# Performance work log

Hardware: AMD Instinct MI355X
Metric: run time of the kernel (lower is better)

Reference implementation:

```python
import jax, jax.numpy as jnp
import numpy as np

B, W, NN, EPG = 8, 16, 64, 1024   # batch, window, nodes/graph, trace-edges/graph
N = B * W * NN                     # 8192 flattened nodes
E = B * W * EPG                    # 131072 node-graph edges == trace rows
E2 = 4 * E                         # 524288 edge-graph (line-graph) edges
D_NODE = 128; D_LOG = 128; D_EDGE = 128
D_IN = D_NODE + D_LOG              # 256 = GATv2 node2node in_channels
H = 4
EPS = 1e-16                        # PyG softmax epsilon


def _lin(key, fan_in, fan_out):
    return jax.random.normal(key, (fan_in, fan_out), jnp.float32) * (1.0 / np.sqrt(fan_in))


def setup_inputs() -> dict:
    key = jax.random.key(0)
    ks = jax.random.split(key, 16)
    return {
        "x_node": jax.random.normal(ks[0], (B, W, NN, D_NODE), jnp.float32),
        "x_trace": jax.random.normal(ks[1], (B, W, EPG, D_EDGE), jnp.float32),
        "x_log": jax.random.normal(ks[2], (B, W, NN, D_LOG), jnp.float32),
        "node_adj": jax.random.randint(ks[3], (2, E), 0, N, jnp.int32),
        "edge_adj": jax.random.randint(ks[4], (2, E2), 0, E, jnp.int32),
        "edge_efea": jax.random.randint(ks[5], (E2,), 0, N, jnp.int32),
        # node2node GATv2Conv: in=256, heads=4, out/head=64, edge_dim=128
        "n2n_Wl": _lin(ks[6], D_IN, D_IN), "n2n_bl": jnp.zeros((D_IN,), jnp.float32),
        "n2n_Wr": _lin(ks[7], D_IN, D_IN), "n2n_br": jnp.zeros((D_IN,), jnp.float32),
        "n2n_We": _lin(ks[8], D_EDGE, D_IN),
        "n2n_att": jax.random.normal(ks[9], (H, D_IN // H), jnp.float32) * 0.1,
        "n2n_bias": jnp.zeros((D_IN,), jnp.float32),
        # egde2node GATv2Conv: in=128, heads=4, out/head=32, edge_dim=256
        "e2n_Wl": _lin(ks[10], D_EDGE, D_EDGE), "e2n_bl": jnp.zeros((D_EDGE,), jnp.float32),
        "e2n_Wr": _lin(ks[11], D_EDGE, D_EDGE), "e2n_br": jnp.zeros((D_EDGE,), jnp.float32),
        "e2n_We": _lin(ks[12], D_IN, D_EDGE),
        "e2n_att": jax.random.normal(ks[13], (H, D_EDGE // H), jnp.float32) * 0.1,
        "e2n_bias": jnp.zeros((D_EDGE,), jnp.float32),
    }


def gatv2(x, edge_index, edge_attr, Wl, bl, Wr, br, We, att, bias, num_nodes):
    """PyG GATv2Conv (eval mode, add_self_loops=False, concat heads)."""
    heads, C = att.shape
    src, dst = edge_index[0], edge_index[1]
    xl = (x @ Wl + bl).reshape(-1, heads, C)   # source transform [N,H,C]
    xr = (x @ Wr + br).reshape(-1, heads, C)   # target transform [N,H,C]
    e = (edge_attr @ We).reshape(-1, heads, C) # edge transform   [E,H,C]
    m = jax.nn.leaky_relu(xl[src] + xr[dst] + e, 0.2)  # [E,H,C]
    alpha = jnp.einsum('ehc,hc->eh', m, att)           # [E,H]
    amax = jax.ops.segment_max(alpha, dst, num_segments=num_nodes)
    ex = jnp.exp(alpha - amax[dst])
    denom = jax.ops.segment_sum(ex, dst, num_segments=num_nodes)
    a = ex / (denom[dst] + EPS)                        # per-target softmax
    out = jax.ops.segment_sum(a[:, :, None] * xl[src], dst, num_segments=num_nodes)
    return out.reshape(num_nodes, heads * C) + bias


def reference(x_node, x_trace, x_log, node_adj, edge_adj, edge_efea,
              n2n_Wl, n2n_bl, n2n_Wr, n2n_br, n2n_We, n2n_att, n2n_bias,
              e2n_Wl, e2n_bl, e2n_Wr, e2n_br, e2n_We, e2n_att, e2n_bias):
    node = jnp.concatenate([x_node, x_log], axis=-1).reshape(-1, D_IN)  # [N,256]
    trace = x_trace.reshape(-1, D_EDGE)                                 # [E,128]
    node = gatv2(node, node_adj, trace,
                 n2n_Wl, n2n_bl, n2n_Wr, n2n_br, n2n_We, n2n_att, n2n_bias, N)
    trace = gatv2(trace, edge_adj, node[edge_efea],
                  e2n_Wl, e2n_bl, e2n_Wr, e2n_br, e2n_We, e2n_att, e2n_bias, E)
    xn = node[:, :D_NODE].reshape(B, W, NN, D_NODE)
    xt = trace.reshape(B, W, EPG, D_EDGE)
    xlg = node[:, D_NODE:].reshape(B, W, NN, D_LOG)
    return (xn, xt, xlg)
```

## Files before the change

### kernel.cpp

```cpp
#include <hip/hip_runtime.h>
#include <hip/hip_bf16.h>

constexpr int N    = 8192;
constexpr int E    = 131072;
constexpr int E2   = 524288;

constexpr size_t XT_OFF  = (size_t)N * 128;
constexpr size_t XLG_OFF = XT_OFF + (size_t)E * 128;

typedef unsigned short u16;
typedef short s16x8 __attribute__((ext_vector_type(8)));
typedef float f32x4 __attribute__((ext_vector_type(4)));

__device__ __forceinline__ u16 f2bs(float f) {
    unsigned x = __float_as_uint(f);
    return (u16)((x + 0x7FFF + ((x >> 16) & 1)) >> 16);
}
__device__ __forceinline__ float bs2f(u16 u) {
    return __uint_as_float((unsigned)u << 16);
}

__global__ __launch_bounds__(256) void k_prep(
    const float* __restrict__ Wl, const float* __restrict__ Wr,
    const float* __restrict__ We, const float* __restrict__ Wl2,
    const float* __restrict__ Wr2, const float* __restrict__ We2,
    u16* __restrict__ Wlt, u16* __restrict__ Wrt, u16* __restrict__ Wet,
    u16* __restrict__ Wl2t, u16* __restrict__ Wr2t, u16* __restrict__ We2t)
{
    const int gid = blockIdx.x * 256 + threadIdx.x;
    const float* src; u16* dst; int base, Kk, sh, perm;
    if      (gid <  65536) { src = Wl;  dst = Wlt;  base = 0;      Kk = 256; sh = 8; perm = 0; }
    else if (gid < 131072) { src = Wr;  dst = Wrt;  base = 65536;  Kk = 256; sh = 8; perm = 0; }
    else if (gid < 163840) { src = We;  dst = Wet;  base = 131072; Kk = 128; sh = 8; perm = 1; }
    else if (gid < 180224) { src = Wl2; dst = Wl2t; base = 163840; Kk = 128; sh = 7; perm = 1; }
    else if (gid < 196608) { src = Wr2; dst = Wr2t; base = 180224; Kk = 128; sh = 7; perm = 1; }
    else                   { src = We2; dst = We2t; base = 196608; Kk = 256; sh = 7; perm = 0; }
    const int l = gid - base;
    const int k = l >> sh, nn = l & ((1 << sh) - 1);
    int ns = nn;
    if (perm) ns = (nn & ~63) | ((nn & 3) << 4) | ((nn >> 2) & 15);
    dst[(size_t)ns * Kk + k] = f2bs(src[l]);
}

__global__ void k_hist(const int* __restrict__ dst, int* __restrict__ cnt, int nE)
{
    int i = blockIdx.x * 256 + threadIdx.x;
    if (i < nE) atomicAdd(&cnt[dst[i]], 1);
}

__global__ __launch_bounds__(1024) void k_scan(
    const int* __restrict__ cnt, int* __restrict__ off, int* __restrict__ cur, int n)
{
    __shared__ int tile[8192];
    __shared__ int wsum[16];
    const int tid = threadIdx.x, lane = tid & 63, wv = tid >> 6;
    int carry = 0;
    for (int base = 0; base < n; base += 8192) {
        for (int i = tid; i < 8192; i += 1024) tile[i] = cnt[base + i];
        __syncthreads();
        const int st = tid * 8;
        int s = 0;
        for (int k = 0; k < 8; ++k) { int v = tile[st + k]; tile[st + k] = s; s += v; }
        const int tsum = s;
        int incl = s;
        for (int o = 1; o < 64; o <<= 1) {
            int v = __shfl_up(incl, o);
            if (lane >= o) incl += v;
        }
        if (lane == 63) wsum[wv] = incl;
        __syncthreads();
        int woff = 0;
        for (int wq = 0; wq < wv; ++wq) woff += wsum[wq];
        int tot = 0;
        for (int wq = 0; wq < 16; ++wq) tot += wsum[wq];
        const int add = carry + woff + incl - tsum;
        for (int k = 0; k < 8; ++k) {
            int o2 = add + tile[st + k];
            off[base + st + k] = o2;
            cur[base + st + k] = o2;
        }
        carry += tot;
        __syncthreads();
    }
    if (tid == 0) off[n] = carry;
}

__global__ void k_scatter1(const int* __restrict__ adj, int* __restrict__ cur,
                           int* __restrict__ srcc, int* __restrict__ pos1, int nE)
{
    int i = blockIdx.x * 256 + threadIdx.x;
    if (i < nE) {
        int pos = atomicAdd(&cur[adj[nE + i]], 1);
        srcc[pos] = adj[i];
        pos1[i] = pos;
    }
}

__global__ void k_scatter2(const int* __restrict__ eadj, const int* __restrict__ efea,
                           int* __restrict__ cur, int2* __restrict__ sf2, int nE)
{
    int i = blockIdx.x * 256 + threadIdx.x;
    if (i < nE) {
        int pos = atomicAdd(&cur[eadj[nE + i]], 1);
        sf2[pos] = make_int2(eadj[i], efea[i]);
    }
}

__global__ __launch_bounds__(256) void k_node_gemm(
    const float* __restrict__ x_node, const float* __restrict__ x_log,
    const u16* __restrict__ Wlt, const float* __restrict__ bl,
    const u16* __restrict__ Wrt, const float* __restrict__ br,
    u16* __restrict__ xl, u16* __restrict__ xr)
{
    __shared__ u16 A[32][260];
    const int n0 = blockIdx.x * 32;
    const int tid = threadIdx.x;
    for (int i = tid; i < 32 * 64; i += 256) {
        const int r = i >> 6, k4 = (i & 63) << 2;
        const float* srcp = (k4 < 128) ? &x_node[(size_t)(n0 + r) * 128 + k4]
                                       : &x_log [(size_t)(n0 + r) * 128 + (k4 - 128)];
        const float4 v = *(const float4*)srcp;
        ushort4 o; o.x = f2bs(v.x); o.y = f2bs(v.y); o.z = f2bs(v.z); o.w = f2bs(v.w);
        *(ushort4*)&A[r][k4] = o;
    }
    __syncthreads();
    const int w = tid >> 6, lane = tid & 63, lr = lane & 15, lq = lane >> 4;
    const u16* Wt     = (w < 2) ? Wlt : Wrt;
    const float* bias = (w < 2) ? bl : br;
    u16* outp         = (w < 2) ? xl : xr;
    const int cb = (w & 1) * 128;
    f32x4 acc[2][8] = {};
    for (int kb = 0; kb < 8; ++kb) {
        s16x8 afr0 = *(const s16x8*)&A[lr][kb * 32 + lq * 8];
        s16x8 afr1 = *(const s16x8*)&A[16 + lr][kb * 32 + lq * 8];
#pragma unroll
        for (int ct = 0; ct < 8; ++ct) {
            const int n = cb + ct * 16 + lr;
            s16x8 bfr = *(const s16x8*)&Wt[(size_t)n * 256 + kb * 32 + lq * 8];
            acc[0][ct] = __builtin_amdgcn_mfma_f32_16x16x32_bf16(afr0, bfr, acc[0][ct], 0, 0, 0);
            acc[1][ct] = __builtin_amdgcn_mfma_f32_16x16x32_bf16(afr1, bfr, acc[1][ct], 0, 0, 0);
        }
    }
#pragma unroll
    for (int rt = 0; rt < 2; ++rt)
#pragma unroll
        for (int ct = 0; ct < 8; ++ct) {
            const int col = cb + ct * 16 + lr;
            const float bv = bias[col];
#pragma unroll
            for (int reg = 0; reg < 4; ++reg) {
                const int row = n0 + rt * 16 + lq * 4 + reg;
                outp[(size_t)row * 256 + col] = f2bs(acc[rt][ct][reg] + bv);
            }
        }
}

__global__ __launch_bounds__(512) void k_edge_mm(
    const float* __restrict__ x_trace,
    const int* __restrict__ adj,
    const int* __restrict__ pos1,
    const u16* __restrict__ xl_n, const u16* __restrict__ xr_n,
    const u16* __restrict__ Wet,
    const u16* __restrict__ Wl2t, const float* __restrict__ bl2,
    const u16* __restrict__ Wr2t, const float* __restrict__ br2,
    const float* __restrict__ att,
    float* __restrict__ alpha, u16* __restrict__ xl_e, u16* __restrict__ xrst)
{
    __shared__ u16 A[32][132];
    __shared__ int ss[32], dd[32], pp[32];
    const int e0 = blockIdx.x * 32;
    const int tid = threadIdx.x;
    for (int i = tid; i < 32 * 32; i += 512) {
        const int r = i >> 5, k4 = (i & 31) << 2;
        const float4 v = *(const float4*)&x_trace[(size_t)(e0 + r) * 128 + k4];
        ushort4 o; o.x = f2bs(v.x); o.y = f2bs(v.y); o.z = f2bs(v.z); o.w = f2bs(v.w);
        *(ushort4*)&A[r][k4] = o;
    }
    if (tid < 32) {
        ss[tid] = adj[e0 + tid];
        dd[tid] = adj[E + e0 + tid];
        pp[tid] = pos1[e0 + tid];
    }
    __syncthreads();
    const int w8 = tid >> 6;
    const int role = w8 >> 2;
    const int w = w8 & 3;
    const int lane = tid & 63, lr = lane & 15, lq = lane >> 4;

    if (role == 0) {
        const int co = w * 64 + lr * 4;
        ushort4 xlv[2][4], xrv[2][4];
#pragma unroll
        for (int rt = 0; rt < 2; ++rt)
#pragma unroll
            for (int reg = 0; reg < 4; ++reg) {
                const int rowt = rt * 16 + lq * 4 + reg;
                xlv[rt][reg] = *(const ushort4*)&xl_n[(size_t)ss[rowt] * 256 + co];
                xrv[rt][reg] = *(const ushort4*)&xr_n[(size_t)dd[rowt] * 256 + co];
            }
        f32x4 acc1[2][4] = {};
        for (int kb = 0; kb < 4; ++kb) {
            s16x8 afr0 = *(const s16x8*)&A[lr][kb * 32 + lq * 8];
            s16x8 afr1 = *(const s16x8*)&A[16 + lr][kb * 32 + lq * 8];
#pragma unroll
            for (int ct = 0; ct < 4; ++ct) {
                const int n1 = w * 64 + ct * 16 + lr;
                s16x8 bfr = *(const s16x8*)&Wet[(size_t)n1 * 128 + kb * 32 + lq * 8];
                acc1[0][ct] = __builtin_amdgcn_mfma_f32_16x16x32_bf16(afr0, bfr, acc1[0][ct], 0, 0, 0);
                acc1[1][ct] = __builtin_amdgcn_mfma_f32_16x16x32_bf16(afr1, bfr, acc1[1][ct], 0, 0, 0);
            }
        }
        const float4 attq = *(const float4*)&att[w * 64 + lr * 4];
        float sums[2][4];
#pragma unroll
        for (int rt = 0; rt < 2; ++rt)
#pragma unroll
            for (int reg = 0; reg < 4; ++reg) {
                float m0 = acc1[rt][0][reg] + bs2f(xlv[rt][reg].x) + bs2f(xrv[rt][reg].x);
                float m1 = acc1[rt][1][reg] + bs2f(xlv[rt][reg].y) + bs2f(xrv[rt][reg].y);
                float m2 = acc1[rt][2][reg] + bs2f(xlv[rt][reg].z) + bs2f(xrv[rt][reg].z);
                float m3 = acc1[rt][3][reg] + bs2f(xlv[rt][reg].w) + bs2f(xrv[rt][reg].w);
                m0 = m0 > 0.f ? m0 : 0.2f * m0;
                m1 = m1 > 0.f ? m1 : 0.2f * m1;
                m2 = m2 > 0.f ? m2 : 0.2f * m2;
                m3 = m3 > 0.f ? m3 : 0.2f * m3;
                sums[rt][reg] = m0 * attq.x + m1 * attq.y + m2 * attq.z + m3 * attq.w;
            }
#pragma unroll
        for (int rt = 0; rt < 2; ++rt)
#pragma unroll
            for (int reg = 0; reg < 4; ++reg) {
                float p = sums[rt][reg];
                p += __shfl_xor(p, 8);
                p += __shfl_xor(p, 4);
                p += __shfl_xor(p, 2);
                p += __shfl_xor(p, 1);
                if (lr == 0)
                    alpha[(size_t)pp[rt * 16 + lq * 4 + reg] * 4 + w] = p;
            }
    } else {
        const u16* Wt2  = (w < 2) ? Wl2t : Wr2t;
        const float* b2 = (w < 2) ? bl2 : br2;
        const int cb2 = (w & 1) * 64;
        f32x4 acc2[2][4] = {};
        for (int kb = 0; kb < 4; ++kb) {
            s16x8 afr0 = *(const s16x8*)&A[lr][kb * 32 + lq * 8];
            s16x8 afr1 = *(const s16x8*)&A[16 + lr][kb * 32 + lq * 8];
#pragma unroll
            for (int ct = 0; ct < 4; ++ct) {
                const int n2 = cb2 + ct * 16 + lr;
                s16x8 bfr = *(const s16x8*)&Wt2[(size_t)n2 * 128 + kb * 32 + lq * 8];
                acc2[0][ct] = __builtin_amdgcn_mfma_f32_16x16x32_bf16(afr0, bfr, acc2[0][ct], 0, 0, 0);
                acc2[1][ct] = __builtin_amdgcn_mfma_f32_16x16x32_bf16(afr1, bfr, acc2[1][ct], 0, 0, 0);
            }
        }
        const float4 b2q = *(const float4*)&b2[cb2 + lr * 4];
#pragma unroll
        for (int rt = 0; rt < 2; ++rt)
#pragma unroll
            for (int reg = 0; reg < 4; ++reg) {
                const int row = e0 + rt * 16 + lq * 4 + reg;
                ushort4 o;
                o.x = f2bs(acc2[rt][0][reg] + b2q.x);
                o.y = f2bs(acc2[rt][1][reg] + b2q.y);
                o.z = f2bs(acc2[rt][2][reg] + b2q.z);
                o.w = f2bs(acc2[rt][3][reg] + b2q.w);
                if (w < 2) *(ushort4*)&xl_e[(size_t)row * 128 + cb2 + lr * 4] = o;
                else       *(ushort4*)&xrst[(size_t)row * 256 + cb2 + lr * 4] = o;
            }
    }
}

__global__ __launch_bounds__(256) void k_fused1(
    const int* __restrict__ off, const int* __restrict__ srcc,
    const float* __restrict__ alphac,
    const u16* __restrict__ xl,
    const float* __restrict__ bias,
    float* __restrict__ out)
{
    const int wv = __builtin_amdgcn_readfirstlane(threadIdx.x >> 6);
    const int lane = threadIdx.x & 63;
    const int n = blockIdx.x * 4 + wv;
    const int c = lane * 4;
    const int h = lane >> 4;
    const int beg = off[n], end = off[n + 1];
    float mx = -INFINITY, den = 0.f;
    float a0 = 0.f, a1 = 0.f, a2 = 0.f, a3 = 0.f;
    int i = beg;
    while (i < end) {
        const int rem = end - i;
        int sa[8]; float pe[8];
#pragma unroll
        for (int k = 0; k < 8; ++k) {
            const int idx = i + (k < rem ? k : rem - 1);
            sa[k] = srcc[idx];
            pe[k] = alphac[(size_t)idx * 4 + h];
        }
        ushort4 xv[8];
#pragma unroll
        for (int k = 0; k < 8; ++k)
            xv[k] = *(const ushort4*)&xl[(size_t)sa[k] * 256 + c];
#pragma unroll
        for (int k = 0; k < 8; ++k) {
            const float p = (k < rem) ? pe[k] : -INFINITY;
            const float mnew = fmaxf(mx, p);
            const float sc = __expf(mx - mnew);
            const float ex = __expf(p - mnew);
            den = den * sc + ex;
            a0 = a0 * sc + ex * bs2f(xv[k].x);
            a1 = a1 * sc + ex * bs2f(xv[k].y);
            a2 = a2 * sc + ex * bs2f(xv[k].z);
            a3 = a3 * sc + ex * bs2f(xv[k].w);
            mx = mnew;
        }
        i += 8;
    }
    const float inv = 1.f / (den + 1e-16f);
    float4 r;
    r.x = a0 * inv + bias[c + 0];
    r.y = a1 * inv + bias[c + 1];
    r.z = a2 * inv + bias[c + 2];
    r.w = a3 * inv + bias[c + 3];
    if (lane < 32) *(float4*)&out[(size_t)n * 128 + c] = r;
    else           *(float4*)&out[XLG_OFF + (size_t)n * 128 + (c - 128)] = r;
}

__global__ __launch_bounds__(256) void k_proj_gemm(
    const float* __restrict__ out_node, const u16* __restrict__ We2t,
    u16* __restrict__ proj)
{
    __shared__ u16 A[32][260];
    const int n0 = blockIdx.x * 32;
    const int tid = threadIdx.x;
    for (int i = tid; i < 32 * 64; i += 256) {
        const int r = i >> 6, k4 = (i & 63) << 2;
        const float* srcp = (k4 < 128)
            ? &out_node[(size_t)(n0 + r) * 128 + k4]
            : &out_node[XLG_OFF + (size_t)(n0 + r) * 128 + (k4 - 128)];
        const float4 v = *(const float4*)srcp;
        ushort4 o; o.x = f2bs(v.x); o.y = f2bs(v.y); o.z = f2bs(v.z); o.w = f2bs(v.w);
        *(ushort4*)&A[r][k4] = o;
    }
    __syncthreads();
    const int w = tid >> 6, lane = tid & 63, lr = lane & 15, lq = lane >> 4;
    f32x4 acc[2][2] = {};
    for (int kb = 0; kb < 8; ++kb) {
        s16x8 afr0 = *(const s16x8*)&A[lr][kb * 32 + lq * 8];
        s16x8 afr1 = *(const s16x8*)&A[16 + lr][kb * 32 + lq * 8];
#pragma unroll
        for (int ct = 0; ct < 2; ++ct) {
            const int col = w * 32 + ct * 16 + lr;
            s16x8 bfr = *(const s16x8*)&We2t[(size_t)col * 256 + kb * 32 + lq * 8];
            acc[0][ct] = __builtin_amdgcn_mfma_f32_16x16x32_bf16(afr0, bfr, acc[0][ct], 0, 0, 0);
            acc[1][ct] = __builtin_amdgcn_mfma_f32_16x16x32_bf16(afr1, bfr, acc[1][ct], 0, 0, 0);
        }
    }
#pragma unroll
    for (int rt = 0; rt < 2; ++rt)
#pragma unroll
        for (int ct = 0; ct < 2; ++ct) {
            const int col = w * 32 + ct * 16 + lr;
#pragma unroll
            for (int reg = 0; reg < 4; ++reg) {
                const int row = n0 + rt * 16 + lq * 4 + reg;
                proj[(size_t)row * 128 + col] = f2bs(acc[rt][ct][reg]);
            }
        }
}

__global__ __launch_bounds__(256) void k_fused2(
    const int* __restrict__ off, const int2* __restrict__ sf2,
    const u16* __restrict__ xl,
    const u16* __restrict__ proj,
    const float* __restrict__ att,
    const float* __restrict__ bias,
    float* __restrict__ out)
{
    const int wv = __builtin_amdgcn_readfirstlane(threadIdx.x >> 6);
    const int lane = threadIdx.x & 63;
    const int d = blockIdx.x * 4 + wv;
    const int c = lane * 2;
    const u16* xrst = (const u16*)(out + XT_OFF);
    const unsigned xrp = *(const unsigned*)&xrst[(size_t)d * 256 + c];
    const float xr0 = bs2f((u16)(xrp & 0xffff));
    const float xr1 = bs2f((u16)(xrp >> 16));
    const float av0 = att[c], av1 = att[c + 1];
    const int beg = off[d], end = off[d + 1];
    float mx = -INFINITY, den = 0.f, a0 = 0.f, a1 = 0.f;
    int i = beg;
    while (i < end) {
        const int rem = end - i;
        int2 sf[4];
#pragma unroll
        for (int k = 0; k < 4; ++k) sf[k] = sf2[i + (k < rem ? k : rem - 1)];
        unsigned xv[4], pv[4];
#pragma unroll
        for (int k = 0; k < 4; ++k) {
            xv[k] = *(const unsigned*)&xl[(size_t)sf[k].x * 128 + c];
            pv[k] = *(const unsigned*)&proj[(size_t)sf[k].y * 128 + c];
        }
#pragma unroll
        for (int k = 0; k < 4; ++k) {
            const float x0 = bs2f((u16)(xv[k] & 0xffff));
            const float x1 = bs2f((u16)(xv[k] >> 16));
            float m0 = x0 + xr0 + bs2f((u16)(pv[k] & 0xffff));
            float m1 = x1 + xr1 + bs2f((u16)(pv[k] >> 16));
            m0 = m0 > 0.f ? m0 : 0.2f * m0;
            m1 = m1 > 0.f ? m1 : 0.2f * m1;
            float pp = m0 * av0 + m1 * av1;
            pp += __shfl_xor(pp, 8, 16);
            pp += __shfl_xor(pp, 4, 16);
            pp += __shfl_xor(pp, 2, 16);
            pp += __shfl_xor(pp, 1, 16);
            const float p = (k < rem) ? pp : -INFINITY;
            const float mnew = fmaxf(mx, p);
            const float sc = __expf(mx - mnew);
            const float ex = __expf(p - mnew);
            den = den * sc + ex;
            a0 = a0 * sc + ex * x0;
            a1 = a1 * sc + ex * x1;
            mx = mnew;
        }
        i += 4;
    }
    const float inv = 1.f / (den + 1e-16f);
    float2 o2;
    o2.x = a0 * inv + bias[c];
    o2.y = a1 * inv + bias[c + 1];
    *(float2*)&out[XT_OFF + (size_t)d * 128 + c] = o2;
}

extern "C" void kernel_launch(void* const* d_in, const int* in_sizes, int n_in,
                              void* d_out, int out_size, void* d_ws, size_t ws_size,
                              hipStream_t stream)
{
    const float* x_node   = (const float*)d_in[0];
    const float* x_trace  = (const float*)d_in[1];
    const float* x_log    = (const float*)d_in[2];
    const int*   node_adj = (const int*)d_in[3];
    const int*   edge_adj = (const int*)d_in[4];
    const int*   efea     = (const int*)d_in[5];
    const float* n2n_Wl   = (const float*)d_in[6];
    const float* n2n_bl   = (const float*)d_in[7];
    const float* n2n_Wr   = (const float*)d_in[8];
    const float* n2n_br   = (const float*)d_in[9];
    const float* n2n_We   = (const float*)d_in[10];
    const float* n2n_att  = (const float*)d_in[11];
    const float* n2n_bias = (const float*)d_in[12];
    const float* e2n_Wl   = (const float*)d_in[13];
    const float* e2n_bl   = (const float*)d_in[14];
    const float* e2n_Wr   = (const float*)d_in[15];
    const float* e2n_br   = (const float*)d_in[16];
    const float* e2n_We   = (const float*)d_in[17];
    const float* e2n_att  = (const float*)d_in[18];
    const float* e2n_bias = (const float*)d_in[19];
    float* out = (float*)d_out;

    char* w = (char*)d_ws;
    int*  cnt1   = (int*)w;   w += (size_t)N * 4;
    int*  cnt2   = (int*)w;   w += (size_t)E * 4;
    int*  off1   = (int*)w;   w += (size_t)(N + 4) * 4;
    int*  cur1   = (int*)w;   w += (size_t)N * 4;
    int*  src1   = (int*)w;   w += (size_t)E * 4;
    int*  pos1   = (int*)w;   w += (size_t)E * 4;
    float* alphac = (float*)w; w += (size_t)E * 4 * 4;
    int*  off2   = (int*)w;   w += (size_t)(E + 4) * 4;
    int*  cur2   = (int*)w;   w += (size_t)E * 4;
    int2* sf2    = (int2*)w;  w += (size_t)E2 * 8;
    u16*  xl_n   = (u16*)w;   w += (size_t)N * 256 * 2;
    u16*  xr_n   = (u16*)w;   w += (size_t)N * 256 * 2;
    u16*  xl_e   = (u16*)w;   w += (size_t)E * 128 * 2;
    u16*  proj   = (u16*)w;   w += (size_t)N * 128 * 2;
    u16*  Wlt    = (u16*)w;   w += (size_t)65536 * 2;
    u16*  Wrt    = (u16*)w;   w += (size_t)65536 * 2;
    u16*  Wet    = (u16*)w;   w += (size_t)32768 * 2;
    u16*  Wl2t   = (u16*)w;   w += (size_t)16384 * 2;
    u16*  Wr2t   = (u16*)w;   w += (size_t)16384 * 2;
    u16*  We2t   = (u16*)w;   w += (size_t)32768 * 2;

    hipMemsetAsync(d_ws, 0, (size_t)(N + E) * 4, stream);

    k_prep<<<896, 256, 0, stream>>>(n2n_Wl, n2n_Wr, n2n_We, e2n_Wl, e2n_Wr, e2n_We,
                                    Wlt, Wrt, Wet, Wl2t, Wr2t, We2t);
    k_hist<<<E / 256, 256, 0, stream>>>(node_adj + E, cnt1, E);
    k_scan<<<1, 1024, 0, stream>>>(cnt1, off1, cur1, N);
    k_scatter1<<<E / 256, 256, 0, stream>>>(node_adj, cur1, src1, pos1, E);
    k_hist<<<E2 / 256, 256, 0, stream>>>(edge_adj + E2, cnt2, E2);
    k_scan<<<1, 1024, 0, stream>>>(cnt2, off2, cur2, E);
    k_scatter2<<<E2 / 256, 256, 0, stream>>>(edge_adj, efea, cur2, sf2, E2);

    k_node_gemm<<<N / 32, 256, 0, stream>>>(x_node, x_log, Wlt, n2n_bl, Wrt, n2n_br,
                                            xl_n, xr_n);
    k_edge_mm<<<E / 32, 512, 0, stream>>>(x_trace, node_adj, pos1, xl_n, xr_n,
                                          Wet, Wl2t, e2n_bl, Wr2t, e2n_br,
                                          n2n_att, alphac, xl_e, (u16*)(out + XT_OFF));
    k_fused1<<<N / 4, 256, 0, stream>>>(off1, src1, alphac, xl_n, n2n_bias, out);

    k_proj_gemm<<<N / 32, 256, 0, stream>>>(out, We2t, proj);
    k_fused2<<<E / 4, 256, 0, stream>>>(off2, sf2, xl_e, proj,
                                        e2n_att, e2n_bias, out);
}
```

Baseline: 453.8 us.

## Make edge GEMM kernel persistent over 8 tiles with double-buffered LDS and register-cached weights

Each block of k_edge_mm now handles 8 consecutive 32-edge tiles instead of one. The weight fragments are loaded into registers once per block instead of being re-read from global memory for every tile. The next tile's x_trace rows and indices are staged into a second LDS buffer while the current tile computes. This cuts repeated weight traffic and overlaps loads with MFMA work, but the grid shrinks to 512 blocks and register pressure rises from the 64 cached weight vectors per thread.

```diff
diff --git a/kernel.cpp b/kernel.cpp
--- a/kernel.cpp
+++ b/kernel.cpp
@@ -155,6 +155,7 @@
         }
 }
 
+constexpr int TPB_EDGE = 8;
 __global__ __launch_bounds__(512) void k_edge_mm(
     const float* __restrict__ x_trace,
     const int* __restrict__ adj,
@@ -166,108 +167,159 @@
     const float* __restrict__ att,
     float* __restrict__ alpha, u16* __restrict__ xl_e, u16* __restrict__ xrst)
 {
-    __shared__ u16 A[32][132];
-    __shared__ int ss[32], dd[32], pp[32];
-    const int e0 = blockIdx.x * 32;
+    __shared__ u16 A[2][32][132];
+    __shared__ int ss[2][32], dd[2][32], pp[2][32];
     const int tid = threadIdx.x;
-    for (int i = tid; i < 32 * 32; i += 512) {
-        const int r = i >> 5, k4 = (i & 31) << 2;
-        const float4 v = *(const float4*)&x_trace[(size_t)(e0 + r) * 128 + k4];
-        ushort4 o; o.x = f2bs(v.x); o.y = f2bs(v.y); o.z = f2bs(v.z); o.w = f2bs(v.w);
-        *(ushort4*)&A[r][k4] = o;
-    }
-    if (tid < 32) {
-        ss[tid] = adj[e0 + tid];
-        dd[tid] = adj[E + e0 + tid];
-        pp[tid] = pos1[e0 + tid];
-    }
-    __syncthreads();
     const int w8 = tid >> 6;
     const int role = w8 >> 2;
     const int w = w8 & 3;
     const int lane = tid & 63, lr = lane & 15, lq = lane >> 4;
 
+    s16x8 wf[4][4];
+    const int cb2 = (w & 1) * 64;
     if (role == 0) {
-        const int co = w * 64 + lr * 4;
-        ushort4 xlv[2][4], xrv[2][4];
-#pragma unroll
-        for (int rt = 0; rt < 2; ++rt)
-#pragma unroll
-            for (int reg = 0; reg < 4; ++reg) {
-                const int rowt = rt * 16 + lq * 4 + reg;
-                xlv[rt][reg] = *(const ushort4*)&xl_n[(size_t)ss[rowt] * 256 + co];
-                xrv[rt][reg] = *(const ushort4*)&xr_n[(size_t)dd[rowt] * 256 + co];
-            }
-        f32x4 acc1[2][4] = {};
-        for (int kb = 0; kb < 4; ++kb) {
-            s16x8 afr0 = *(const s16x8*)&A[lr][kb * 32 + lq * 8];
-            s16x8 afr1 = *(const s16x8*)&A[16 + lr][kb * 32 + lq * 8];
-#pragma unroll
-            for (int ct = 0; ct < 4; ++ct) {
-                const int n1 = w * 64 + ct * 16 + lr;
-                s16x8 bfr = *(const s16x8*)&Wet[(size_t)n1 * 128 + kb * 32 + lq * 8];
-                acc1[0][ct] = __builtin_amdgcn_mfma_f32_16x16x32_bf16(afr0, bfr, acc1[0][ct], 0, 0, 0);
-                acc1[1][ct] = __builtin_amdgcn_mfma_f32_16x16x32_bf16(afr1, bfr, acc1[1][ct], 0, 0, 0);
-            }
-        }
-        const float4 attq = *(const float4*)&att[w * 64 + lr * 4];
-        float sums[2][4];
-#pragma unroll
-        for (int rt = 0; rt < 2; ++rt)
-#pragma unroll
-            for (int reg = 0; reg < 4; ++reg) {
-                float m0 = acc1[rt][0][reg] + bs2f(xlv[rt][reg].x) + bs2f(xrv[rt][reg].x);
-                float m1 = acc1[rt][1][reg] + bs2f(xlv[rt][reg].y) + bs2f(xrv[rt][reg].y);
-                float m2 = acc1[rt][2][reg] + bs2f(xlv[rt][reg].z) + bs2f(xrv[rt][reg].z);
-                float m3 = acc1[rt][3][reg] + bs2f(xlv[rt][reg].w) + bs2f(xrv[rt][reg].w);
-                m0 = m0 > 0.f ? m0 : 0.2f * m0;
-                m1 = m1 > 0.f ? m1 : 0.2f * m1;
-                m2 = m2 > 0.f ? m2 : 0.2f * m2;
-                m3 = m3 > 0.f ? m3 : 0.2f * m3;
-                sums[rt][reg] = m0 * attq.x + m1 * attq.y + m2 * attq.z + m3 * attq.w;
-            }
-#pragma unroll
-        for (int rt = 0; rt < 2; ++rt)
-#pragma unroll
-            for (int reg = 0; reg < 4; ++reg) {
-                float p = sums[rt][reg];
-                p += __shfl_xor(p, 8);
-                p += __shfl_xor(p, 4);
-                p += __shfl_xor(p, 2);
-                p += __shfl_xor(p, 1);
-                if (lr == 0)
-                    alpha[(size_t)pp[rt * 16 + lq * 4 + reg] * 4 + w] = p;
-            }
+#pragma unroll
+        for (int kb = 0; kb < 4; ++kb)
+#pragma unroll
+            for (int ct = 0; ct < 4; ++ct)
+                wf[kb][ct] = *(const s16x8*)&Wet[(size_t)(w * 64 + ct * 16 + lr) * 128 + kb * 32 + lq * 8];
     } else {
-        const u16* Wt2  = (w < 2) ? Wl2t : Wr2t;
-        const float* b2 = (w < 2) ? bl2 : br2;
-        const int cb2 = (w & 1) * 64;
-        f32x4 acc2[2][4] = {};
-        for (int kb = 0; kb < 4; ++kb) {
-            s16x8 afr0 = *(const s16x8*)&A[lr][kb * 32 + lq * 8];
-            s16x8 afr1 = *(const s16x8*)&A[16 + lr][kb * 32 + lq * 8];
-#pragma unroll
-            for (int ct = 0; ct < 4; ++ct) {
-                const int n2 = cb2 + ct * 16 + lr;
-                s16x8 bfr = *(const s16x8*)&Wt2[(size_t)n2 * 128 + kb * 32 + lq * 8];
-                acc2[0][ct] = __builtin_amdgcn_mfma_f32_16x16x32_bf16(afr0, bfr, acc2[0][ct], 0, 0, 0);
-                acc2[1][ct] = __builtin_amdgcn_mfma_f32_16x16x32_bf16(afr1, bfr, acc2[1][ct], 0, 0, 0);
-            }
-        }
-        const float4 b2q = *(const float4*)&b2[cb2 + lr * 4];
-#pragma unroll
-        for (int rt = 0; rt < 2; ++rt)
-#pragma unroll
-            for (int reg = 0; reg < 4; ++reg) {
-                const int row = e0 + rt * 16 + lq * 4 + reg;
-                ushort4 o;
-                o.x = f2bs(acc2[rt][0][reg] + b2q.x);
-                o.y = f2bs(acc2[rt][1][reg] + b2q.y);
-                o.z = f2bs(acc2[rt][2][reg] + b2q.z);
-                o.w = f2bs(acc2[rt][3][reg] + b2q.w);
-                if (w < 2) *(ushort4*)&xl_e[(size_t)row * 128 + cb2 + lr * 4] = o;
-                else       *(ushort4*)&xrst[(size_t)row * 256 + cb2 + lr * 4] = o;
-            }
+        const u16* Wt2 = (w < 2) ? Wl2t : Wr2t;
+#pragma unroll
+        for (int kb = 0; kb < 4; ++kb)
+#pragma unroll
+            for (int ct = 0; ct < 4; ++ct)
+                wf[kb][ct] = *(const s16x8*)&Wt2[(size_t)(cb2 + ct * 16 + lr) * 128 + kb * 32 + lq * 8];
+    }
+    const float4 attq = *(const float4*)&att[w * 64 + lr * 4];
+    const float4 b2q  = (role == 0) ? make_float4(0, 0, 0, 0)
+        : *(const float4*)&((w < 2) ? bl2 : br2)[cb2 + lr * 4];
+
+    const int tile0 = blockIdx.x * TPB_EDGE;
+    {
+        const int e0s = tile0 * 32;
+        const int i0 = tid, i1 = tid + 512;
+        {
+            const int r = i0 >> 5, k4 = (i0 & 31) << 2;
+            const float4 v = *(const float4*)&x_trace[(size_t)(e0s + r) * 128 + k4];
+            ushort4 o; o.x = f2bs(v.x); o.y = f2bs(v.y); o.z = f2bs(v.z); o.w = f2bs(v.w);
+            *(ushort4*)&A[0][r][k4] = o;
+        }
+        {
+            const int r = i1 >> 5, k4 = (i1 & 31) << 2;
+            const float4 v = *(const float4*)&x_trace[(size_t)(e0s + r) * 128 + k4];
+            ushort4 o; o.x = f2bs(v.x); o.y = f2bs(v.y); o.z = f2bs(v.z); o.w = f2bs(v.w);
+            *(ushort4*)&A[0][r][k4] = o;
+        }
+        if (tid < 32) {
+            ss[0][tid] = adj[e0s + tid];
+            dd[0][tid] = adj[E + e0s + tid];
+            pp[0][tid] = pos1[e0s + tid];
+        }
+    }
+
+    for (int t = 0; t < TPB_EDGE; ++t) {
+        __syncthreads();
+        const int b = t & 1;
+        const int e0 = (tile0 + t) * 32;
+        if (t + 1 < TPB_EDGE) {
+            const int e0s = (tile0 + t + 1) * 32;
+            const int bn = b ^ 1;
+            {
+                const int r = tid >> 5, k4 = (tid & 31) << 2;
+                const float4 v = *(const float4*)&x_trace[(size_t)(e0s + r) * 128 + k4];
+                ushort4 o; o.x = f2bs(v.x); o.y = f2bs(v.y); o.z = f2bs(v.z); o.w = f2bs(v.w);
+                *(ushort4*)&A[bn][r][k4] = o;
+            }
+            {
+                const int i1 = tid + 512;
+                const int r = i1 >> 5, k4 = (i1 & 31) << 2;
+                const float4 v = *(const float4*)&x_trace[(size_t)(e0s + r) * 128 + k4];
+                ushort4 o; o.x = f2bs(v.x); o.y = f2bs(v.y); o.z = f2bs(v.z); o.w = f2bs(v.w);
+                *(ushort4*)&A[bn][r][k4] = o;
+            }
+            if (tid < 32) {
+                ss[bn][tid] = adj[e0s + tid];
+                dd[bn][tid] = adj[E + e0s + tid];
+                pp[bn][tid] = pos1[e0s + tid];
+            }
+        }
+
+        if (role == 0) {
+            const int co = w * 64 + lr * 4;
+            ushort4 xlv[2][4], xrv[2][4];
+#pragma unroll
+            for (int rt = 0; rt < 2; ++rt)
+#pragma unroll
+                for (int reg = 0; reg < 4; ++reg) {
+                    const int rowt = rt * 16 + lq * 4 + reg;
+                    xlv[rt][reg] = *(const ushort4*)&xl_n[(size_t)ss[b][rowt] * 256 + co];
+                    xrv[rt][reg] = *(const ushort4*)&xr_n[(size_t)dd[b][rowt] * 256 + co];
+                }
+            f32x4 acc1[2][4] = {};
+#pragma unroll
+            for (int kb = 0; kb < 4; ++kb) {
+                s16x8 afr0 = *(const s16x8*)&A[b][lr][kb * 32 + lq * 8];
+                s16x8 afr1 = *(const s16x8*)&A[b][16 + lr][kb * 32 + lq * 8];
+#pragma unroll
+                for (int ct = 0; ct < 4; ++ct) {
+                    acc1[0][ct] = __builtin_amdgcn_mfma_f32_16x16x32_bf16(afr0, wf[kb][ct], acc1[0][ct], 0, 0, 0);
+                    acc1[1][ct] = __builtin_amdgcn_mfma_f32_16x16x32_bf16(afr1, wf[kb][ct], acc1[1][ct], 0, 0, 0);
+                }
+            }
+            float sums[2][4];
+#pragma unroll
+            for (int rt = 0; rt < 2; ++rt)
+#pragma unroll
+                for (int reg = 0; reg < 4; ++reg) {
+                    float m0 = acc1[rt][0][reg] + bs2f(xlv[rt][reg].x) + bs2f(xrv[rt][reg].x);
+                    float m1 = acc1[rt][1][reg] + bs2f(xlv[rt][reg].y) + bs2f(xrv[rt][reg].y);
+                    float m2 = acc1[rt][2][reg] + bs2f(xlv[rt][reg].z) + bs2f(xrv[rt][reg].z);
+                    float m3 = acc1[rt][3][reg] + bs2f(xlv[rt][reg].w) + bs2f(xrv[rt][reg].w);
+                    m0 = m0 > 0.f ? m0 : 0.2f * m0;
+                    m1 = m1 > 0.f ? m1 : 0.2f * m1;
+                    m2 = m2 > 0.f ? m2 : 0.2f * m2;
+                    m3 = m3 > 0.f ? m3 : 0.2f * m3;
+                    sums[rt][reg] = m0 * attq.x + m1 * attq.y + m2 * attq.z + m3 * attq.w;
+                }
+#pragma unroll
+            for (int rt = 0; rt < 2; ++rt)
+#pragma unroll
+                for (int reg = 0; reg < 4; ++reg) {
+                    float p = sums[rt][reg];
+                    p += __shfl_xor(p, 8);
+                    p += __shfl_xor(p, 4);
+                    p += __shfl_xor(p, 2);
+                    p += __shfl_xor(p, 1);
+                    if (lr == 0)
+                        alpha[(size_t)pp[b][rt * 16 + lq * 4 + reg] * 4 + w] = p;
+                }
+        } else {
+            f32x4 acc2[2][4] = {};
+#pragma unroll
+            for (int kb = 0; kb < 4; ++kb) {
+                s16x8 afr0 = *(const s16x8*)&A[b][lr][kb * 32 + lq * 8];
+                s16x8 afr1 = *(const s16x8*)&A[b][16 + lr][kb * 32 + lq * 8];
+#pragma unroll
+                for (int ct = 0; ct < 4; ++ct) {
+                    acc2[0][ct] = __builtin_amdgcn_mfma_f32_16x16x32_bf16(afr0, wf[kb][ct], acc2[0][ct], 0, 0, 0);
+                    acc2[1][ct] = __builtin_amdgcn_mfma_f32_16x16x32_bf16(afr1, wf[kb][ct], acc2[1][ct], 0, 0, 0);
+                }
+            }
+#pragma unroll
+            for (int rt = 0; rt < 2; ++rt)
+#pragma unroll
+                for (int reg = 0; reg < 4; ++reg) {
+                    const int row = e0 + rt * 16 + lq * 4 + reg;
+                    ushort4 o;
+                    o.x = f2bs(acc2[rt][0][reg] + b2q.x);
+                    o.y = f2bs(acc2[rt][1][reg] + b2q.y);
+                    o.z = f2bs(acc2[rt][2][reg] + b2q.z);
+                    o.w = f2bs(acc2[rt][3][reg] + b2q.w);
+                    if (w < 2) *(ushort4*)&xl_e[(size_t)row * 128 + cb2 + lr * 4] = o;
+                    else       *(ushort4*)&xrst[(size_t)row * 256 + cb2 + lr * 4] = o;
+                }
+        }
     }
 }
 
@@ -491,7 +543,7 @@
 
     k_node_gemm<<<N / 32, 256, 0, stream>>>(x_node, x_log, Wlt, n2n_bl, Wrt, n2n_br,
                                             xl_n, xr_n);
-    k_edge_mm<<<E / 32, 512, 0, stream>>>(x_trace, node_adj, pos1, xl_n, xr_n,
+    k_edge_mm<<<E / (32 * TPB_EDGE), 512, 0, stream>>>(x_trace, node_adj, pos1, xl_n, xr_n,
                                           Wet, Wl2t, e2n_bl, Wr2t, e2n_br,
                                           n2n_att, alphac, xl_e, (u16*)(out + XT_OFF));
     k_fused1<<<N / 4, 256, 0, stream>>>(off1, src1, alphac, xl_n, n2n_bias, out);
```

Measured after the change: 427.5 us. 1.06x faster.
